# Kernel tuning notes

Hardware: AMD Instinct MI355X
Metric: run time of the kernel (lower is better)

The kernel has to match this reference:

```python
import jax, jax.numpy as jnp
import numpy as np
from jax import lax

IN_CH = 256
NUM_CLASSES = 21
ROI = 7
SCALE = 1.0 / 32
SR = 2  # sampling_ratio
B = 2
NPROP = 128
FH = FW = 32
IMG = 1024
SCORE_THRESH = 0.05
NMS_THRESH = 0.5
MAX_DET = 100


def setup_inputs() -> dict:
    key = jax.random.key(0)
    ks = jax.random.split(key, 10)
    features = jax.random.normal(ks[0], (B, IN_CH, FH, FW), jnp.float32)
    x1 = jax.random.uniform(ks[1], (B, NPROP), minval=0.0, maxval=IMG - 160.0)
    y1 = jax.random.uniform(ks[2], (B, NPROP), minval=0.0, maxval=IMG - 160.0)
    w = jax.random.uniform(ks[3], (B, NPROP), minval=32.0, maxval=160.0)
    h = jax.random.uniform(ks[4], (B, NPROP), minval=32.0, maxval=160.0)
    proposals = jnp.stack([x1, y1, x1 + w, y1 + h], axis=-1)  # [B, NPROP, 4]
    img_sizes = jnp.full((B, 2), IMG, dtype=jnp.int32)  # (h, w)
    feat_dim = IN_CH * ROI * ROI

    def kaiming(k, shape):
        return jax.random.normal(k, shape, jnp.float32) * np.float32(np.sqrt(2.0 / shape[1]))

    W1 = kaiming(ks[5], (1024, feat_dim)); b1 = jnp.zeros((1024,), jnp.float32)
    W2 = kaiming(ks[6], (1024, 1024)); b2 = jnp.zeros((1024,), jnp.float32)
    Wc = jax.random.normal(ks[7], (NUM_CLASSES, 1024), jnp.float32) * 0.01
    bc = jnp.zeros((NUM_CLASSES,), jnp.float32)
    Wb = jax.random.normal(ks[8], (NUM_CLASSES * 4, 1024), jnp.float32) * 0.001
    bb = jnp.zeros((NUM_CLASSES * 4,), jnp.float32)
    return dict(features=features, proposals=proposals, img_sizes=img_sizes,
                W1=W1, b1=b1, W2=W2, b2=b2, Wc=Wc, bc=bc, Wb=Wb, bb=bb)


def roi_align(features, bidx, rois):
    """torchvision-style RoIAlign (aligned=False), spatial_scale=SCALE, sampling_ratio=SR.
    features [B,C,H,W], bidx [N] int, rois [N,4] -> [N, C*ROI*ROI] (channel-major flatten)."""
    Bf, C, H, W = features.shape
    x1 = rois[:, 0] * SCALE; y1 = rois[:, 1] * SCALE
    x2 = rois[:, 2] * SCALE; y2 = rois[:, 3] * SCALE
    rw = jnp.maximum(x2 - x1, 1.0); rh = jnp.maximum(y2 - y1, 1.0)
    bw = rw / ROI; bh = rh / ROI
    # per-bin sample offsets: [ROI, SR]
    g = jnp.arange(ROI, dtype=jnp.float32)[:, None] + (jnp.arange(SR, dtype=jnp.float32)[None, :] + 0.5) / SR
    ys = y1[:, None, None] + g[None] * bh[:, None, None]  # [N, ROI, SR]
    xs = x1[:, None, None] + g[None] * bw[:, None, None]  # [N, ROI, SR]
    y = ys[:, :, :, None, None]  # [N,ph,sy,1,1]
    x = xs[:, None, None, :, :]  # [N,1,1,pw,sx]
    inb = (y >= -1.0) & (y <= H) & (x >= -1.0) & (x <= W)  # [N,ph,sy,pw,sx]
    yc = jnp.clip(y, 0.0, H - 1.0); xc = jnp.clip(x, 0.0, W - 1.0)
    y0f = jnp.floor(yc); x0f = jnp.floor(xc)
    y0 = y0f.astype(jnp.int32); x0 = x0f.astype(jnp.int32)
    y1i = jnp.minimum(y0 + 1, H - 1); x1i = jnp.minimum(x0 + 1, W - 1)
    ly = yc - y0f; lx = xc - x0f
    hy = 1.0 - ly; hx = 1.0 - lx
    b = bidx[:, None, None, None, None]
    # gather four corners: advanced indices broadcast -> [N,ph,sy,pw,sx,C]
    f00 = features[b, :, y0, x0]
    f01 = features[b, :, y0, x1i]
    f10 = features[b, :, y1i, x0]
    f11 = features[b, :, y1i, x1i]
    val = ((hy * hx)[..., None] * f00 + (hy * lx)[..., None] * f01
           + (ly * hx)[..., None] * f10 + (ly * lx)[..., None] * f11)
    val = val * inb[..., None]
    pooled = val.mean(axis=(2, 4))            # [N, ph, pw, C]
    pooled = jnp.transpose(pooled, (0, 3, 1, 2))  # [N, C, ph, pw] (torch layout)
    return pooled.reshape(pooled.shape[0], -1)


def decode_boxes(deltas, props):
    pw = props[..., 2] - props[..., 0]
    ph = props[..., 3] - props[..., 1]
    px = props[..., 0] + pw / 2
    py = props[..., 1] + ph / 2
    cx = px + deltas[..., 0] * pw
    cy = py + deltas[..., 1] * ph
    w = pw * jnp.exp(deltas[..., 2])
    h = ph * jnp.exp(deltas[..., 3])
    return jnp.stack([cx - w / 2, cy - h / 2, cx + w / 2, cy + h / 2], axis=-1)


def nms_fixed(boxes, scores, valid, iou_thresh, max_out):
    """Greedy NMS with fixed shapes. Returns (indices[max_out], ok_mask[max_out])."""
    M = scores.shape[0]
    s = jnp.where(valid, scores, -jnp.inf)
    order = jnp.argsort(-s)
    b = boxes[order]; v = valid[order]
    bx1, by1, bx2, by2 = b[:, 0], b[:, 1], b[:, 2], b[:, 3]
    area = (bx2 - bx1) * (by2 - by1)
    idxs = jnp.arange(M)

    def body(i, keep):
        xi1 = jnp.maximum(bx1[i], bx1); yi1 = jnp.maximum(by1[i], by1)
        xi2 = jnp.minimum(bx2[i], bx2); yi2 = jnp.minimum(by2[i], by2)
        inter = jnp.maximum(xi2 - xi1, 0.0) * jnp.maximum(yi2 - yi1, 0.0)
        iou = inter / (area[i] + area - inter + 1e-9)
        suppress = (iou > iou_thresh) & (idxs > i)
        return jnp.where(keep[i], keep & ~suppress, keep)

    keep = lax.fori_loop(0, M, body, v)
    pos = jnp.where(keep, idxs, M)
    take = jnp.sort(pos)[:max_out]
    ok = take < M
    take = jnp.where(ok, take, 0)
    return order[take], ok


def postprocess_image(probs, reg, props, img_hw):
    Ncls = probs.shape[1]
    scores = probs[:, 1:]                    # [N, C-1] (skip background)
    deltas = reg[:, 1:, :]                   # [N, C-1, 4]
    boxes = decode_boxes(deltas, props[:, None, :])  # [N, C-1, 4]
    h = img_hw[0].astype(boxes.dtype); w = img_hw[1].astype(boxes.dtype)
    boxes = jnp.stack([jnp.clip(boxes[..., 0], 0.0, w), jnp.clip(boxes[..., 1], 0.0, h),
                       jnp.clip(boxes[..., 2], 0.0, w), jnp.clip(boxes[..., 3], 0.0, h)], axis=-1)
    labels = jnp.broadcast_to(jnp.arange(1, Ncls, dtype=jnp.int32)[None, :], scores.shape)
    fb = boxes.reshape(-1, 4); fs = scores.reshape(-1); fl = labels.reshape(-1)
    valid = fs > SCORE_THRESH
    maxc = jnp.max(jnp.where(valid, jnp.max(fb, axis=1), 0.0))
    off = fl.astype(fb.dtype) * (maxc + 1.0)
    zero = jnp.zeros_like(off)
    fb_off = fb + jnp.stack([off, zero, off, zero], axis=-1)
    idx, ok = nms_fixed(fb_off, fs, valid, NMS_THRESH, MAX_DET)
    m = ok.astype(fb.dtype)
    return fb[idx] * m[:, None], fs[idx] * m, fl[idx] * ok.astype(jnp.int32)


def reference(features, proposals, img_sizes, W1, b1, W2, b2, Wc, bc, Wb, bb):
    Bn, NP = proposals.shape[0], proposals.shape[1]
    bidx = jnp.repeat(jnp.arange(Bn, dtype=jnp.int32), NP)
    props_flat = proposals.reshape(-1, 4)
    roi_feats = roi_align(features, bidx, props_flat)       # [N, C*49]
    x = jax.nn.relu(roi_feats @ W1.T + b1)
    x = jax.nn.relu(x @ W2.T + b2)
    cls_logits = x @ Wc.T + bc                              # [N, NUM_CLASSES]
    box_reg = (x @ Wb.T + bb).reshape(-1, NUM_CLASSES, 4)   # [N, NUM_CLASSES, 4]
    probs = jax.nn.softmax(cls_logits, axis=-1)
    out_b, out_s, out_l = [], [], []
    for i in range(Bn):
        p = probs[i * NP:(i + 1) * NP]
        r = box_reg[i * NP:(i + 1) * NP]
        bi, si, li = postprocess_image(p, r, proposals[i], img_sizes[i])
        out_b.append(bi); out_s.append(si); out_l.append(li)
    return jnp.stack(out_b), jnp.stack(out_s), jnp.stack(out_l)
```

## Files before the change

kernel.cpp:

```cpp
#include <hip/hip_runtime.h>
#include <math.h>

#define IN_CH   256
#define NCLS    21
#define ROIW    7
#define NPROP   128
#define BATCH   2
#define NROI    (BATCH*NPROP)
#define FEAT_DIM (IN_CH*ROIW*ROIW)
#define HID     1024
#define NCAND   (NPROP*(NCLS-1))
#define MAXDET  100
#define SCORE_T 0.05f
#define NMS_T   0.5f

__global__ __launch_bounds__(256) void transpose_feat(const float* __restrict__ feat,
                                                      float* __restrict__ ft) {
    int img = blockIdx.z;
    int cb = blockIdx.y;
    int pb = blockIdx.x;
    __shared__ float t[32][33];
    int tx = threadIdx.x & 31, ty = threadIdx.x >> 5;
#pragma unroll
    for (int i = 0; i < 4; ++i) {
        int c = ty + i * 8;
        t[c][tx] = feat[(size_t)img * 262144 + (size_t)(cb * 32 + c) * 1024 + pb * 32 + tx];
    }
    __syncthreads();
#pragma unroll
    for (int i = 0; i < 4; ++i) {
        int p = ty + i * 8;
        ft[(size_t)img * 262144 + (size_t)(pb * 32 + p) * 256 + cb * 32 + tx] = t[tx][p];
    }
}

__global__ __launch_bounds__(256) void roi_align_tr(const float* __restrict__ ft,
                                                    const float* __restrict__ props,
                                                    float* __restrict__ out) {
    int n = blockIdx.x >> 1;
    int half = blockIdx.x & 1;
    int img = n / NPROP;
    int q0 = half ? 25 : 0;
    int nq = half ? 24 : 25;
    const float* pr = props + n * 4;
    float x1 = pr[0] * 0.03125f, y1 = pr[1] * 0.03125f;
    float x2 = pr[2] * 0.03125f, y2 = pr[3] * 0.03125f;
    float rw = fmaxf(x2 - x1, 1.0f), rh = fmaxf(y2 - y1, 1.0f);
    float bw = rw / 7.0f, bh = rh / 7.0f;
    int cg = threadIdx.x & 63;
    int qg = threadIdx.x >> 6;
    __shared__ float tile[25][260];
    const float* base = ft + (size_t)img * 262144 + cg * 4;
    for (int j = qg; j < nq; j += 4) {
        int q = q0 + j;
        int iy = q / 7, ix = q % 7;
        float ax = 0.f, ay = 0.f, az = 0.f, aw = 0.f;
#pragma unroll
        for (int s = 0; s < 4; ++s) {
            int sy = s >> 1, sx = s & 1;
            float gy = (float)iy + ((float)sy + 0.5f) / 2.0f;
            float gx = (float)ix + ((float)sx + 0.5f) / 2.0f;
            float y = y1 + gy * bh;
            float x = x1 + gx * bw;
            bool inb = (y >= -1.0f) && (y <= 32.0f) && (x >= -1.0f) && (x <= 32.0f);
            float yc = fminf(fmaxf(y, 0.0f), 31.0f);
            float xc = fminf(fmaxf(x, 0.0f), 31.0f);
            float y0f = floorf(yc), x0f = floorf(xc);
            int y0 = (int)y0f, x0i = (int)x0f;
            int y1i = min(y0 + 1, 31), x1i = min(x0i + 1, 31);
            float ly = yc - y0f, lx = xc - x0f;
            float hy = 1.0f - ly, hx = 1.0f - lx;
            float wg = inb ? 1.0f : 0.0f;
            float w00 = hy * hx * wg, w01 = hy * lx * wg, w10 = ly * hx * wg, w11 = ly * lx * wg;
            float4 f00 = *(const float4*)(base + (size_t)(y0 * 32 + x0i) * 256);
            float4 f01 = *(const float4*)(base + (size_t)(y0 * 32 + x1i) * 256);
            float4 f10 = *(const float4*)(base + (size_t)(y1i * 32 + x0i) * 256);
            float4 f11 = *(const float4*)(base + (size_t)(y1i * 32 + x1i) * 256);
            ax += w00 * f00.x + w01 * f01.x + w10 * f10.x + w11 * f11.x;
            ay += w00 * f00.y + w01 * f01.y + w10 * f10.y + w11 * f11.y;
            az += w00 * f00.z + w01 * f01.z + w10 * f10.z + w11 * f11.z;
            aw += w00 * f00.w + w01 * f01.w + w10 * f10.w + w11 * f11.w;
        }
        *(float4*)&tile[j][cg * 4] = make_float4(ax * 0.25f, ay * 0.25f, az * 0.25f, aw * 0.25f);
    }
    __syncthreads();
    float* ob = out + (size_t)n * FEAT_DIM + q0;
    int tid = threadIdx.x;
    if (half == 0) {
        for (int i = tid; i < 256 * 25; i += 256) {
            int c = i / 25, ql = i % 25;
            ob[c * 49 + ql] = tile[ql][c];
        }
    } else {
        for (int i = tid; i < 256 * 24; i += 256) {
            int c = i / 24, ql = i % 24;
            ob[c * 49 + ql] = tile[ql][c];
        }
    }
}

#define GBM 128
#define GBN 128
#define GBK 16
__global__ __launch_bounds__(256) void gemm_tn_part(const float* __restrict__ A,
                                                    const float* __restrict__ Wt,
                                                    float* __restrict__ Cp,
                                                    int Nr, int Mo, int K) {
    const int S = gridDim.z;
    const int kchunk = K / S;
    const int k0 = blockIdx.z * kchunk;
    const int n0 = blockIdx.y * GBM;
    const int j0 = blockIdx.x * GBN;
    __shared__ float As[GBK][GBM + 4];
    __shared__ float Ws[GBK][GBN + 4];
    const int tid = threadIdx.x;
    const int tx = tid & 15;
    const int ty = tid >> 4;
    const int r0 = tx << 2;
    const int c0 = ty << 2;
    const int srow = tid >> 1;
    const int skk = (tid & 1) << 3;
    float acc[8][8];
#pragma unroll
    for (int r = 0; r < 8; ++r)
#pragma unroll
        for (int c = 0; c < 8; ++c) acc[r][c] = 0.0f;

    const int iters = kchunk / GBK;
    const float* Abase = A + (size_t)(n0 + srow) * K + skk;
    const float* Wbase = Wt + (size_t)(j0 + srow) * K + skk;
    float4 pa0 = *(const float4*)(Abase + k0);
    float4 pa1 = *(const float4*)(Abase + k0 + 4);
    float4 pw0 = *(const float4*)(Wbase + k0);
    float4 pw1 = *(const float4*)(Wbase + k0 + 4);

#pragma unroll 1
    for (int it = 0; it < iters; ++it) {
        __syncthreads();
        As[skk + 0][srow] = pa0.x; As[skk + 1][srow] = pa0.y; As[skk + 2][srow] = pa0.z; As[skk + 3][srow] = pa0.w;
        As[skk + 4][srow] = pa1.x; As[skk + 5][srow] = pa1.y; As[skk + 6][srow] = pa1.z; As[skk + 7][srow] = pa1.w;
        Ws[skk + 0][srow] = pw0.x; Ws[skk + 1][srow] = pw0.y; Ws[skk + 2][srow] = pw0.z; Ws[skk + 3][srow] = pw0.w;
        Ws[skk + 4][srow] = pw1.x; Ws[skk + 5][srow] = pw1.y; Ws[skk + 6][srow] = pw1.z; Ws[skk + 7][srow] = pw1.w;
        __syncthreads();
        if (it + 1 < iters) {
            int kc = k0 + (it + 1) * GBK;
            pa0 = *(const float4*)(Abase + kc);
            pa1 = *(const float4*)(Abase + kc + 4);
            pw0 = *(const float4*)(Wbase + kc);
            pw1 = *(const float4*)(Wbase + kc + 4);
        }
        float4 fa0[2], fa1[2], fw0[2], fw1[2];
        fa0[0] = *(const float4*)&As[0][r0];
        fa1[0] = *(const float4*)&As[0][r0 + 64];
        fw0[0] = *(const float4*)&Ws[0][c0];
        fw1[0] = *(const float4*)&Ws[0][c0 + 64];
#pragma unroll
        for (int k = 0; k < GBK; ++k) {
            const int cur = k & 1, nxt = cur ^ 1;
            if (k + 1 < GBK) {
                fa0[nxt] = *(const float4*)&As[k + 1][r0];
                fa1[nxt] = *(const float4*)&As[k + 1][r0 + 64];
                fw0[nxt] = *(const float4*)&Ws[k + 1][c0];
                fw1[nxt] = *(const float4*)&Ws[k + 1][c0 + 64];
            }
            float a[8] = {fa0[cur].x, fa0[cur].y, fa0[cur].z, fa0[cur].w,
                          fa1[cur].x, fa1[cur].y, fa1[cur].z, fa1[cur].w};
            float w[8] = {fw0[cur].x, fw0[cur].y, fw0[cur].z, fw0[cur].w,
                          fw1[cur].x, fw1[cur].y, fw1[cur].z, fw1[cur].w};
#pragma unroll
            for (int r = 0; r < 8; ++r)
#pragma unroll
                for (int c = 0; c < 8; ++c)
                    acc[r][c] = fmaf(a[r], w[c], acc[r][c]);
        }
    }
#pragma unroll
    for (int r = 0; r < 8; ++r) {
        int gr = n0 + ((r < 4) ? (r0 + r) : (r0 + 64 + r - 4));
        float* o = Cp + ((size_t)blockIdx.z * Nr + gr) * Mo + j0;
        *(float4*)(o + c0)      = make_float4(acc[r][0], acc[r][1], acc[r][2], acc[r][3]);
        *(float4*)(o + c0 + 64) = make_float4(acc[r][4], acc[r][5], acc[r][6], acc[r][7]);
    }
}

__global__ __launch_bounds__(256) void reduce_bias_relu(const float* __restrict__ Cp,
                                                        const float* __restrict__ bias,
                                                        float* __restrict__ X,
                                                        int Nr, int Mo, int S) {
    int idx = blockIdx.x * 256 + threadIdx.x;
    int total = (Nr * Mo) >> 2;
    if (idx >= total) return;
    int e = idx << 2;
    int j = e % Mo;
    float4 s = make_float4(0.f, 0.f, 0.f, 0.f);
    for (int ss = 0; ss < S; ++ss) {
        float4 c = *(const float4*)(Cp + (size_t)ss * Nr * Mo + e);
        s.x += c.x; s.y += c.y; s.z += c.z; s.w += c.w;
    }
    float4 b = *(const float4*)(bias + j);
    s.x = fmaxf(s.x + b.x, 0.f); s.y = fmaxf(s.y + b.y, 0.f);
    s.z = fmaxf(s.z + b.z, 0.f); s.w = fmaxf(s.w + b.w, 0.f);
    *(float4*)(X + e) = s;
}

__global__ __launch_bounds__(256) void heads_cand_k(const float* __restrict__ Cp2,
                                                    const float* __restrict__ b2,
                                                    const float* __restrict__ Wc, const float* __restrict__ bc,
                                                    const float* __restrict__ Wb, const float* __restrict__ bb,
                                                    const float* __restrict__ props,
                                                    const int* __restrict__ img_sizes,
                                                    float* __restrict__ cbox,
                                                    float* __restrict__ csc,
                                                    unsigned long long* __restrict__ ckey,
                                                    int* __restrict__ vcount) {
    int n = blockIdx.x;
    int tid = threadIdx.x;
    if (n == 0 && tid < 2) vcount[tid] = 0;
    __shared__ float xs[HID];
    __shared__ float lg[NCLS];
    __shared__ float bs[84];
    __shared__ float ssum;
    {
        int e = n * HID + tid * 4;
        float4 s = make_float4(0.f, 0.f, 0.f, 0.f);
#pragma unroll
        for (int ss = 0; ss < 16; ++ss) {
            float4 c = *(const float4*)(Cp2 + (size_t)ss * (NROI * HID) + e);
            s.x += c.x; s.y += c.y; s.z += c.z; s.w += c.w;
        }
        float4 b = *(const float4*)(b2 + tid * 4);
        s.x = fmaxf(s.x + b.x, 0.f); s.y = fmaxf(s.y + b.y, 0.f);
        s.z = fmaxf(s.z + b.z, 0.f); s.w = fmaxf(s.w + b.w, 0.f);
        *(float4*)&xs[tid * 4] = s;
    }
    __syncthreads();
    int wave = tid >> 6, lane = tid & 63;
    for (int h = wave; h < 105; h += 4) {
        const float* w = (h < 21) ? (Wc + (size_t)h * HID) : (Wb + (size_t)(h - 21) * HID);
        float acc = 0.0f;
#pragma unroll
        for (int k0 = 0; k0 < HID; k0 += 256) {
            float4 wv = *(const float4*)(w + k0 + lane * 4);
            float4 xv = *(const float4*)&xs[k0 + lane * 4];
            acc = fmaf(wv.x, xv.x, acc);
            acc = fmaf(wv.y, xv.y, acc);
            acc = fmaf(wv.z, xv.z, acc);
            acc = fmaf(wv.w, xv.w, acc);
        }
#pragma unroll
        for (int m = 32; m; m >>= 1) acc += __shfl_xor(acc, m, 64);
        if (lane == 0) {
            if (h < 21) lg[h] = acc + bc[h];
            else bs[h - 21] = acc + bb[h - 21];
        }
    }
    __syncthreads();
    if (tid == 0) {
        float m = lg[0];
        for (int c = 1; c < 21; ++c) m = fmaxf(m, lg[c]);
        float s = 0.0f;
        for (int c = 0; c < 21; ++c) { float e = expf(lg[c] - m); lg[c] = e; s += e; }
        ssum = s;
    }
    __syncthreads();
    if (tid < 20) {
        int c = tid + 1;
        int img = n / NPROP;
        float s = lg[c] / ssum;
        const float* pr = props + n * 4;
        float pw = pr[2] - pr[0], ph = pr[3] - pr[1];
        float px = pr[0] + pw * 0.5f, py = pr[1] + ph * 0.5f;
        const float* d = &bs[c * 4];
        float cx = px + d[0] * pw;
        float cy = py + d[1] * ph;
        float w = pw * expf(d[2]);
        float h = ph * expf(d[3]);
        float bx1 = cx - w * 0.5f, by1 = cy - h * 0.5f, bx2 = cx + w * 0.5f, by2 = cy + h * 0.5f;
        float Wi = (float)img_sizes[img * 2 + 1], Hi = (float)img_sizes[img * 2 + 0];
        bx1 = fminf(fmaxf(bx1, 0.f), Wi); by1 = fminf(fmaxf(by1, 0.f), Hi);
        bx2 = fminf(fmaxf(bx2, 0.f), Wi); by2 = fminf(fmaxf(by2, 0.f), Hi);
        int t = n * 20 + tid;
        *(float4*)(cbox + (size_t)t * 4) = make_float4(bx1, by1, bx2, by2);
        csc[t] = s;
        bool valid = s > SCORE_T;
        unsigned int sb = __float_as_uint(s);
        int m = t - img * NCAND;
        ckey[t] = valid ? (((unsigned long long)sb << 32) | (unsigned int)(NCAND - 1 - m)) : 0ull;
    }
}

__global__ __launch_bounds__(256) void rank_k(const float* __restrict__ cbox,
                                              const float* __restrict__ csc,
                                              const unsigned long long* __restrict__ ckey,
                                              float* __restrict__ sbox, float* __restrict__ ssc,
                                              int* __restrict__ sm, int* __restrict__ vcount) {
    int img = blockIdx.x / 40;
    int seg = blockIdx.x % 40;
    int base = img * NCAND;
    int lm = threadIdx.x & 63;
    int chunk = threadIdx.x >> 6;
    int m = seg * 64 + lm;
    __shared__ __align__(16) unsigned long long keys[NCAND];
    for (int j = threadIdx.x; j < NCAND; j += 256) keys[j] = ckey[base + j];
    unsigned long long mykey = ckey[base + m];
    float s = csc[base + m];
    bool valid = s > SCORE_T;
    __syncthreads();
    const ulonglong2* kp = (const ulonglong2*)&keys[chunk * 640];
    int r = 0;
#pragma unroll 4
    for (int j = 0; j < 320; ++j) {
        ulonglong2 kk = kp[j];
        r += (kk.x > mykey) ? 1 : 0;
        r += (kk.y > mykey) ? 1 : 0;
    }
    __shared__ int part[4][64];
    part[chunk][lm] = r;
    __syncthreads();
    if (chunk == 0) {
        int rank = part[0][lm] + part[1][lm] + part[2][lm] + part[3][lm];
        if (valid) {
            int o = base + rank;
            *(float4*)(sbox + (size_t)o * 4) = *(const float4*)(cbox + (size_t)(base + m) * 4);
            ssc[o] = s;
            sm[o] = m;
        }
    }
    int cnt = __syncthreads_count((chunk == 0) && valid);
    if (threadIdx.x == 0) atomicAdd(&vcount[img], cnt);
}

__global__ __launch_bounds__(64) void nms_k(const int* __restrict__ sm,
                                            const float* __restrict__ sbox,
                                            const int* __restrict__ vcount,
                                            int* __restrict__ skeep) {
    int bid = blockIdx.x;
    int img = bid / 20;
    int cls = bid % 20 + 1;
    int V = vcount[img];
    __shared__ float lx1[128], ly1[128], lx2[128], ly2[128];
    __shared__ int lpos[128];
    __shared__ int lcnt;
    __shared__ int keepL[128];
    int lane = threadIdx.x;
    if (lane == 0) lcnt = 0;
    __syncthreads();
    for (int p0 = 0; p0 < V; p0 += 64) {
        int p = p0 + lane;
        bool pred = false;
        if (p < V) {
            int m = sm[img * NCAND + p];
            pred = (m % 20 + 1) == cls;
        }
        unsigned long long mask = __ballot(pred);
        int base = lcnt;
        if (pred) {
            int idx = base + __popcll(mask & ((1ull << lane) - 1ull));
            const float* bx = sbox + (size_t)(img * NCAND + (p0 + lane)) * 4;
            lx1[idx] = bx[0]; ly1[idx] = bx[1]; lx2[idx] = bx[2]; ly2[idx] = bx[3];
            lpos[idx] = p0 + lane;
        }
        __syncthreads();
        if (lane == 0) lcnt += (int)__popcll(mask);
        __syncthreads();
    }
    int C = lcnt;
    for (int j = lane; j < 128; j += 64) keepL[j] = 1;
    __syncthreads();
    for (int i = 0; i < C; ++i) {
        __syncthreads();
        if (keepL[i] == 0) continue;
        float X1 = lx1[i], Y1 = ly1[i], X2 = lx2[i], Y2 = ly2[i];
        float ai = (X2 - X1) * (Y2 - Y1);
        for (int j = i + 1 + lane; j < C; j += 64) {
            if (keepL[j]) {
                float xi1 = fmaxf(X1, lx1[j]);
                float yi1 = fmaxf(Y1, ly1[j]);
                float xi2 = fminf(X2, lx2[j]);
                float yi2 = fminf(Y2, ly2[j]);
                float inter = fmaxf(xi2 - xi1, 0.f) * fmaxf(yi2 - yi1, 0.f);
                float aj = (lx2[j] - lx1[j]) * (ly2[j] - ly1[j]);
                float iou = inter / (ai + aj - inter + 1e-9f);
                if (iou > NMS_T) keepL[j] = 0;
            }
        }
    }
    __syncthreads();
    for (int j = lane; j < C; j += 64) skeep[img * NCAND + lpos[j]] = keepL[j];
}

__global__ __launch_bounds__(256) void write_k(const float* __restrict__ sbox,
                                               const float* __restrict__ ssc,
                                               const int* __restrict__ sm,
                                               const int* __restrict__ skeep,
                                               const int* __restrict__ vcount,
                                               float* __restrict__ out) {
    int img = blockIdx.x;
    int tid = threadIdx.x;
    float* ob = out + img * MAXDET * 4;
    float* os = out + BATCH * MAXDET * 4 + img * MAXDET;
    float* ol = out + BATCH * MAXDET * 5 + img * MAXDET;
    for (int i = tid; i < MAXDET * 4; i += 256) ob[i] = 0.0f;
    for (int i = tid; i < MAXDET; i += 256) { os[i] = 0.0f; ol[i] = 0.0f; }
    __syncthreads();
    int V = vcount[img];
    int chunk = (V + 255) / 256;
    int lo = tid * chunk, hi = min(lo + chunk, V);
    int cnt = 0;
    for (int p = lo; p < hi; ++p) cnt += skeep[img * NCAND + p];
    __shared__ int cs[256];
    __shared__ int pre[256];
    cs[tid] = cnt;
    __syncthreads();
    if (tid == 0) {
        int run = 0;
        for (int t = 0; t < 256; ++t) { pre[t] = run; run += cs[t]; }
    }
    __syncthreads();
    int r = pre[tid];
    for (int p = lo; p < hi; ++p) {
        if (skeep[img * NCAND + p]) {
            if (r < MAXDET) {
                const float* bx = sbox + (size_t)(img * NCAND + p) * 4;
                ob[r * 4 + 0] = bx[0]; ob[r * 4 + 1] = bx[1];
                ob[r * 4 + 2] = bx[2]; ob[r * 4 + 3] = bx[3];
                os[r] = ssc[img * NCAND + p];
                ol[r] = (float)(sm[img * NCAND + p] % 20 + 1);
            }
            ++r;
        }
    }
}

extern "C" void kernel_launch(void* const* d_in, const int* in_sizes, int n_in,
                              void* d_out, int out_size, void* d_ws, size_t ws_size,
                              hipStream_t stream) {
    const float* features  = (const float*)d_in[0];
    const float* proposals = (const float*)d_in[1];
    const int*   img_sizes = (const int*)d_in[2];
    const float* W1 = (const float*)d_in[3];
    const float* b1 = (const float*)d_in[4];
    const float* W2 = (const float*)d_in[5];
    const float* b2 = (const float*)d_in[6];
    const float* Wc = (const float*)d_in[7];
    const float* bc = (const float*)d_in[8];
    const float* Wb = (const float*)d_in[9];
    const float* bb = (const float*)d_in[10];
    float* out = (float*)d_out;

    float* ws = (float*)d_ws;
    float* roi   = ws;
    float* x1    = roi + 3211264;
    float* cpart = x1 + 262144;
    float* featT = cpart;
    float* cbox  = cpart + 16 * 262144;
    float* csc   = cbox + 20480;
    unsigned long long* ckey = (unsigned long long*)(csc + 5120);
    float* sbox  = csc + 5120 + 10240;
    float* ssc   = sbox + 20480;
    int*   sm    = (int*)(ssc + 5120);
    int*   skeep = sm + 5120;
    int*   vcnt  = skeep + 5120;

    hipLaunchKernelGGL(transpose_feat, dim3(32, 8, 2), dim3(256), 0, stream, features, featT);
    hipLaunchKernelGGL(roi_align_tr, dim3(NROI * 2), dim3(256), 0, stream, featT, proposals, roi);
    hipLaunchKernelGGL(gemm_tn_part, dim3(8, 2, 16), dim3(256), 0, stream, roi, W1, cpart, NROI, HID, FEAT_DIM);
    hipLaunchKernelGGL(reduce_bias_relu, dim3(256), dim3(256), 0, stream, cpart, b1, x1, NROI, HID, 16);
    hipLaunchKernelGGL(gemm_tn_part, dim3(8, 2, 16), dim3(256), 0, stream, x1, W2, cpart, NROI, HID, HID);
    hipLaunchKernelGGL(heads_cand_k, dim3(NROI), dim3(256), 0, stream, cpart, b2, Wc, bc, Wb, bb,
                       proposals, img_sizes, cbox, csc, ckey, vcnt);
    hipLaunchKernelGGL(rank_k, dim3(80), dim3(256), 0, stream, cbox, csc, ckey, sbox, ssc, sm, vcnt);
    hipLaunchKernelGGL(nms_k, dim3(BATCH * 20), dim3(64), 0, stream, sm, sbox, vcnt, skeep);
    hipLaunchKernelGGL(write_k, dim3(BATCH), dim3(256), 0, stream, sbox, ssc, sm, skeep, vcnt, out);
}
```

Measured before the change: 319.9 us.

## Replace LDS-tiled GEMM with register-direct K-major GEMM using transposed activations

Activations are transposed to K-major layout (a new transpose kernel for the RoI features, and the reduce/bias/ReLU kernel now writes its output transposed). The GEMM then drops shared memory and barriers entirely: each thread loads its A fragments straight from global memory as float4 and its W rows as float4 runs of 4 k-values. This removes LDS traffic and syncs, but adds an extra pass over the 12.8MB RoI tensor. It also relies on L1/L2 for reuse, since each thread's strided W row reads are uncoalesced across the wave and A reads are repeated across blocks.

```diff
diff --git a/kernel.cpp b/kernel.cpp
--- a/kernel.cpp
+++ b/kernel.cpp
@@ -31,6 +31,25 @@
     for (int i = 0; i < 4; ++i) {
         int p = ty + i * 8;
         ft[(size_t)img * 262144 + (size_t)(pb * 32 + p) * 256 + cb * 32 + tx] = t[tx][p];
+    }
+}
+
+__global__ __launch_bounds__(256) void transpose_mat(const float* __restrict__ in,
+                                                     float* __restrict__ out,
+                                                     int R, int C) {
+    __shared__ float t[32][33];
+    int cb = blockIdx.x * 32, rb = blockIdx.y * 32;
+    int tx = threadIdx.x & 31, ty = threadIdx.x >> 5;
+#pragma unroll
+    for (int i = 0; i < 4; ++i) {
+        int r = rb + ty + i * 8;
+        t[ty + i * 8][tx] = in[(size_t)r * C + cb + tx];
+    }
+    __syncthreads();
+#pragma unroll
+    for (int i = 0; i < 4; ++i) {
+        int c = cb + ty + i * 8;
+        out[(size_t)c * R + rb + tx] = t[tx][ty + i * 8];
     }
 }
 
@@ -99,74 +118,49 @@
     }
 }
 
-#define GBM 128
-#define GBN 128
-#define GBK 16
-__global__ __launch_bounds__(256) void gemm_tn_part(const float* __restrict__ A,
-                                                    const float* __restrict__ Wt,
-                                                    float* __restrict__ Cp,
-                                                    int Nr, int Mo, int K) {
+__global__ __launch_bounds__(256) void gemm_kt(const float* __restrict__ At,
+                                               const float* __restrict__ W,
+                                               float* __restrict__ Cp,
+                                               int Nr, int Mo, int K) {
     const int S = gridDim.z;
     const int kchunk = K / S;
     const int k0 = blockIdx.z * kchunk;
-    const int n0 = blockIdx.y * GBM;
-    const int j0 = blockIdx.x * GBN;
-    __shared__ float As[GBK][GBM + 4];
-    __shared__ float Ws[GBK][GBN + 4];
+    const int n0 = blockIdx.y * 128;
+    const int j0 = blockIdx.x * 128;
     const int tid = threadIdx.x;
     const int tx = tid & 15;
     const int ty = tid >> 4;
     const int r0 = tx << 2;
     const int c0 = ty << 2;
-    const int srow = tid >> 1;
-    const int skk = (tid & 1) << 3;
     float acc[8][8];
 #pragma unroll
     for (int r = 0; r < 8; ++r)
 #pragma unroll
         for (int c = 0; c < 8; ++c) acc[r][c] = 0.0f;
 
-    const int iters = kchunk / GBK;
-    const float* Abase = A + (size_t)(n0 + srow) * K + skk;
-    const float* Wbase = Wt + (size_t)(j0 + srow) * K + skk;
-    float4 pa0 = *(const float4*)(Abase + k0);
-    float4 pa1 = *(const float4*)(Abase + k0 + 4);
-    float4 pw0 = *(const float4*)(Wbase + k0);
-    float4 pw1 = *(const float4*)(Wbase + k0 + 4);
+    const float* a_base = At + (size_t)k0 * Nr + n0 + r0;
+    const float* w0base = W + (size_t)(j0 + c0) * K + k0;
+    const float* w1base = W + (size_t)(j0 + c0 + 64) * K + k0;
+    const int runs = kchunk >> 2;
 
 #pragma unroll 1
-    for (int it = 0; it < iters; ++it) {
-        __syncthreads();
-        As[skk + 0][srow] = pa0.x; As[skk + 1][srow] = pa0.y; As[skk + 2][srow] = pa0.z; As[skk + 3][srow] = pa0.w;
-        As[skk + 4][srow] = pa1.x; As[skk + 5][srow] = pa1.y; As[skk + 6][srow] = pa1.z; As[skk + 7][srow] = pa1.w;
-        Ws[skk + 0][srow] = pw0.x; Ws[skk + 1][srow] = pw0.y; Ws[skk + 2][srow] = pw0.z; Ws[skk + 3][srow] = pw0.w;
-        Ws[skk + 4][srow] = pw1.x; Ws[skk + 5][srow] = pw1.y; Ws[skk + 6][srow] = pw1.z; Ws[skk + 7][srow] = pw1.w;
-        __syncthreads();
-        if (it + 1 < iters) {
-            int kc = k0 + (it + 1) * GBK;
-            pa0 = *(const float4*)(Abase + kc);
-            pa1 = *(const float4*)(Abase + kc + 4);
-            pw0 = *(const float4*)(Wbase + kc);
-            pw1 = *(const float4*)(Wbase + kc + 4);
-        }
-        float4 fa0[2], fa1[2], fw0[2], fw1[2];
-        fa0[0] = *(const float4*)&As[0][r0];
-        fa1[0] = *(const float4*)&As[0][r0 + 64];
-        fw0[0] = *(const float4*)&Ws[0][c0];
-        fw1[0] = *(const float4*)&Ws[0][c0 + 64];
-#pragma unroll
-        for (int k = 0; k < GBK; ++k) {
-            const int cur = k & 1, nxt = cur ^ 1;
-            if (k + 1 < GBK) {
-                fa0[nxt] = *(const float4*)&As[k + 1][r0];
-                fa1[nxt] = *(const float4*)&As[k + 1][r0 + 64];
-                fw0[nxt] = *(const float4*)&Ws[k + 1][c0];
-                fw1[nxt] = *(const float4*)&Ws[k + 1][c0 + 64];
-            }
-            float a[8] = {fa0[cur].x, fa0[cur].y, fa0[cur].z, fa0[cur].w,
-                          fa1[cur].x, fa1[cur].y, fa1[cur].z, fa1[cur].w};
-            float w[8] = {fw0[cur].x, fw0[cur].y, fw0[cur].z, fw0[cur].w,
-                          fw1[cur].x, fw1[cur].y, fw1[cur].z, fw1[cur].w};
+    for (int run = 0; run < runs; ++run) {
+        float4 wr[8];
+#pragma unroll
+        for (int c = 0; c < 4; ++c) {
+            wr[c]     = *(const float4*)(w0base + (size_t)c * K + run * 4);
+            wr[c + 4] = *(const float4*)(w1base + (size_t)c * K + run * 4);
+        }
+#pragma unroll
+        for (int k = 0; k < 4; ++k) {
+            const float* ap = a_base + (size_t)(run * 4 + k) * Nr;
+            float4 a0 = *(const float4*)(ap);
+            float4 a1 = *(const float4*)(ap + 64);
+            float a[8] = {a0.x, a0.y, a0.z, a0.w, a1.x, a1.y, a1.z, a1.w};
+            float w[8];
+#pragma unroll
+            for (int c = 0; c < 8; ++c)
+                w[c] = (k == 0) ? wr[c].x : (k == 1) ? wr[c].y : (k == 2) ? wr[c].z : wr[c].w;
 #pragma unroll
             for (int r = 0; r < 8; ++r)
 #pragma unroll
@@ -183,24 +177,27 @@
     }
 }
 
-__global__ __launch_bounds__(256) void reduce_bias_relu(const float* __restrict__ Cp,
-                                                        const float* __restrict__ bias,
-                                                        float* __restrict__ X,
-                                                        int Nr, int Mo, int S) {
-    int idx = blockIdx.x * 256 + threadIdx.x;
-    int total = (Nr * Mo) >> 2;
-    if (idx >= total) return;
-    int e = idx << 2;
-    int j = e % Mo;
-    float4 s = make_float4(0.f, 0.f, 0.f, 0.f);
-    for (int ss = 0; ss < S; ++ss) {
-        float4 c = *(const float4*)(Cp + (size_t)ss * Nr * Mo + e);
-        s.x += c.x; s.y += c.y; s.z += c.z; s.w += c.w;
-    }
-    float4 b = *(const float4*)(bias + j);
-    s.x = fmaxf(s.x + b.x, 0.f); s.y = fmaxf(s.y + b.y, 0.f);
-    s.z = fmaxf(s.z + b.z, 0.f); s.w = fmaxf(s.w + b.w, 0.f);
-    *(float4*)(X + e) = s;
+__global__ __launch_bounds__(256) void reduce_bias_relu_t(const float* __restrict__ Cp,
+                                                          const float* __restrict__ bias,
+                                                          float* __restrict__ XT,
+                                                          int Nr, int Mo, int S) {
+    __shared__ float t[32][33];
+    int jb = blockIdx.x * 32, nb = blockIdx.y * 32;
+    int tx = threadIdx.x & 31, ty = threadIdx.x >> 5;
+#pragma unroll
+    for (int i = 0; i < 4; ++i) {
+        int nl = ty + i * 8;
+        int e = (nb + nl) * Mo + jb + tx;
+        float s = 0.0f;
+        for (int ss = 0; ss < S; ++ss) s += Cp[(size_t)ss * Nr * Mo + e];
+        t[nl][tx] = fmaxf(s + bias[jb + tx], 0.0f);
+    }
+    __syncthreads();
+#pragma unroll
+    for (int i = 0; i < 4; ++i) {
+        int jl = ty + i * 8;
+        XT[(size_t)(jb + jl) * Nr + nb + tx] = t[tx][jl];
+    }
 }
 
 __global__ __launch_bounds__(256) void heads_cand_k(const float* __restrict__ Cp2,
@@ -450,8 +447,9 @@
 
     float* ws = (float*)d_ws;
     float* roi   = ws;
-    float* x1    = roi + 3211264;
-    float* cpart = x1 + 262144;
+    float* roiT  = roi + 3211264;
+    float* x1T   = roiT + 3211264;
+    float* cpart = x1T + 262144;
     float* featT = cpart;
     float* cbox  = cpart + 16 * 262144;
     float* csc   = cbox + 20480;
@@ -464,9 +462,12 @@
 
     hipLaunchKernelGGL(transpose_feat, dim3(32, 8, 2), dim3(256), 0, stream, features, featT);
     hipLaunchKernelGGL(roi_align_tr, dim3(NROI * 2), dim3(256), 0, stream, featT, proposals, roi);
-    hipLaunchKernelGGL(gemm_tn_part, dim3(8, 2, 16), dim3(256), 0, stream, roi, W1, cpart, NROI, HID, FEAT_DIM);
-    hipLaunchKernelGGL(reduce_bias_relu, dim3(256), dim3(256), 0, stream, cpart, b1, x1, NROI, HID, 16);
-    hipLaunchKernelGGL(gemm_tn_part, dim3(8, 2, 16), dim3(256), 0, stream, x1, W2, cpart, NROI, HID, HID);
+    hipLaunchKernelGGL(transpose_mat, dim3(FEAT_DIM / 32, NROI / 32), dim3(256), 0, stream,
+                       roi, roiT, NROI, FEAT_DIM);
+    hipLaunchKernelGGL(gemm_kt, dim3(8, 2, 16), dim3(256), 0, stream, roiT, W1, cpart, NROI, HID, FEAT_DIM);
+    hipLaunchKernelGGL(reduce_bias_relu_t, dim3(HID / 32, NROI / 32), dim3(256), 0, stream,
+                       cpart, b1, x1T, NROI, HID, 16);
+    hipLaunchKernelGGL(gemm_kt, dim3(8, 2, 16), dim3(256), 0, stream, x1T, W2, cpart, NROI, HID, HID);
     hipLaunchKernelGGL(heads_cand_k, dim3(NROI), dim3(256), 0, stream, cpart, b2, Wc, bc, Wb, bb,
                        proposals, img_sizes, cbox, csc, ckey, vcnt);
     hipLaunchKernelGGL(rank_k, dim3(80), dim3(256), 0, stream, cbox, csc, ckey, sbox, ssc, sm, vcnt);
```

Result: slower. 686.5 us (+114.6%).

## Add 256-row FC1 GEMM kernel so W1 is read once, raise split-K to 28

Applied to the files above, without the earlier changes.

Adds a dedicated FC1 GEMM kernel whose block covers all 256 ROI rows and 128 output columns with a 16x8 per-thread accumulator. Each W1 tile is then loaded once instead of once per 128-row block, which halves W1 global traffic. Split-K goes from 16 to 28 (K=12544 divides into 448-element chunks) to keep 224 blocks in flight and fill the GPU. The trade-off is higher register pressure from 128 accumulators, launch_bounds(256,1), and more partial sums for the reduce kernel to read. The shared-memory register double-buffering in the generic GEMM is also removed.

```diff
diff --git a/kernel.cpp b/kernel.cpp
--- a/kernel.cpp
+++ b/kernel.cpp
@@ -13,6 +13,7 @@
 #define MAXDET  100
 #define SCORE_T 0.05f
 #define NMS_T   0.5f
+#define S_FC1   28
 
 __global__ __launch_bounds__(256) void transpose_feat(const float* __restrict__ feat,
                                                       float* __restrict__ ft) {
@@ -99,6 +100,87 @@
     }
 }
 
+#define G2K 16
+__global__ __launch_bounds__(256, 1) void gemm_fc1(const float* __restrict__ A,
+                                                   const float* __restrict__ Wt,
+                                                   float* __restrict__ Cp,
+                                                   int Nr, int Mo, int K) {
+    const int S = gridDim.y;
+    const int kchunk = K / S;
+    const int k0 = blockIdx.y * kchunk;
+    const int j0 = blockIdx.x * 128;
+    __shared__ float As[G2K][256 + 4];
+    __shared__ float Ws[G2K][128 + 4];
+    const int tid = threadIdx.x;
+    const int tx = tid & 15;
+    const int ty = tid >> 4;
+    const int r0 = tx << 2;
+    const int c0 = ty << 2;
+    const int rA = tid;
+    const int rW = tid >> 1;
+    const int kW = (tid & 1) << 3;
+    float acc[16][8];
+#pragma unroll
+    for (int r = 0; r < 16; ++r)
+#pragma unroll
+        for (int c = 0; c < 8; ++c) acc[r][c] = 0.0f;
+
+    const int iters = kchunk / G2K;
+    const float* Ab = A + (size_t)rA * K;
+    const float* Wb = Wt + (size_t)(j0 + rW) * K + kW;
+    float4 pa0 = *(const float4*)(Ab + k0);
+    float4 pa1 = *(const float4*)(Ab + k0 + 4);
+    float4 pa2 = *(const float4*)(Ab + k0 + 8);
+    float4 pa3 = *(const float4*)(Ab + k0 + 12);
+    float4 pw0 = *(const float4*)(Wb + k0);
+    float4 pw1 = *(const float4*)(Wb + k0 + 4);
+
+#pragma unroll 1
+    for (int it = 0; it < iters; ++it) {
+        __syncthreads();
+        As[0][rA] = pa0.x;  As[1][rA] = pa0.y;  As[2][rA] = pa0.z;  As[3][rA] = pa0.w;
+        As[4][rA] = pa1.x;  As[5][rA] = pa1.y;  As[6][rA] = pa1.z;  As[7][rA] = pa1.w;
+        As[8][rA] = pa2.x;  As[9][rA] = pa2.y;  As[10][rA] = pa2.z; As[11][rA] = pa2.w;
+        As[12][rA] = pa3.x; As[13][rA] = pa3.y; As[14][rA] = pa3.z; As[15][rA] = pa3.w;
+        Ws[kW + 0][rW] = pw0.x; Ws[kW + 1][rW] = pw0.y; Ws[kW + 2][rW] = pw0.z; Ws[kW + 3][rW] = pw0.w;
+        Ws[kW + 4][rW] = pw1.x; Ws[kW + 5][rW] = pw1.y; Ws[kW + 6][rW] = pw1.z; Ws[kW + 7][rW] = pw1.w;
+        __syncthreads();
+        if (it + 1 < iters) {
+            int kc = k0 + (it + 1) * G2K;
+            pa0 = *(const float4*)(Ab + kc);
+            pa1 = *(const float4*)(Ab + kc + 4);
+            pa2 = *(const float4*)(Ab + kc + 8);
+            pa3 = *(const float4*)(Ab + kc + 12);
+            pw0 = *(const float4*)(Wb + kc);
+            pw1 = *(const float4*)(Wb + kc + 4);
+        }
+#pragma unroll
+        for (int k = 0; k < G2K; ++k) {
+            float4 a0 = *(const float4*)&As[k][r0];
+            float4 a1 = *(const float4*)&As[k][r0 + 64];
+            float4 a2 = *(const float4*)&As[k][r0 + 128];
+            float4 a3 = *(const float4*)&As[k][r0 + 192];
+            float4 u0 = *(const float4*)&Ws[k][c0];
+            float4 u1 = *(const float4*)&Ws[k][c0 + 64];
+            float a[16] = {a0.x, a0.y, a0.z, a0.w, a1.x, a1.y, a1.z, a1.w,
+                           a2.x, a2.y, a2.z, a2.w, a3.x, a3.y, a3.z, a3.w};
+            float w[8] = {u0.x, u0.y, u0.z, u0.w, u1.x, u1.y, u1.z, u1.w};
+#pragma unroll
+            for (int r = 0; r < 16; ++r)
+#pragma unroll
+                for (int c = 0; c < 8; ++c)
+                    acc[r][c] = fmaf(a[r], w[c], acc[r][c]);
+        }
+    }
+#pragma unroll
+    for (int r = 0; r < 16; ++r) {
+        int gr = r0 + (r >> 2) * 64 + (r & 3);
+        float* o = Cp + ((size_t)blockIdx.y * Nr + gr) * Mo + j0;
+        *(float4*)(o + c0)      = make_float4(acc[r][0], acc[r][1], acc[r][2], acc[r][3]);
+        *(float4*)(o + c0 + 64) = make_float4(acc[r][4], acc[r][5], acc[r][6], acc[r][7]);
+    }
+}
+
 #define GBM 128
 #define GBN 128
 #define GBK 16
@@ -149,24 +231,14 @@
             pw0 = *(const float4*)(Wbase + kc);
             pw1 = *(const float4*)(Wbase + kc + 4);
         }
-        float4 fa0[2], fa1[2], fw0[2], fw1[2];
-        fa0[0] = *(const float4*)&As[0][r0];
-        fa1[0] = *(const float4*)&As[0][r0 + 64];
-        fw0[0] = *(const float4*)&Ws[0][c0];
-        fw1[0] = *(const float4*)&Ws[0][c0 + 64];
 #pragma unroll
         for (int k = 0; k < GBK; ++k) {
-            const int cur = k & 1, nxt = cur ^ 1;
-            if (k + 1 < GBK) {
-                fa0[nxt] = *(const float4*)&As[k + 1][r0];
-                fa1[nxt] = *(const float4*)&As[k + 1][r0 + 64];
-                fw0[nxt] = *(const float4*)&Ws[k + 1][c0];
-                fw1[nxt] = *(const float4*)&Ws[k + 1][c0 + 64];
-            }
-            float a[8] = {fa0[cur].x, fa0[cur].y, fa0[cur].z, fa0[cur].w,
-                          fa1[cur].x, fa1[cur].y, fa1[cur].z, fa1[cur].w};
-            float w[8] = {fw0[cur].x, fw0[cur].y, fw0[cur].z, fw0[cur].w,
-                          fw1[cur].x, fw1[cur].y, fw1[cur].z, fw1[cur].w};
+            float4 t0 = *(const float4*)&As[k][r0];
+            float4 t1 = *(const float4*)&As[k][r0 + 64];
+            float4 u0 = *(const float4*)&Ws[k][c0];
+            float4 u1 = *(const float4*)&Ws[k][c0 + 64];
+            float a[8] = {t0.x, t0.y, t0.z, t0.w, t1.x, t1.y, t1.z, t1.w};
+            float w[8] = {u0.x, u0.y, u0.z, u0.w, u1.x, u1.y, u1.z, u1.w};
 #pragma unroll
             for (int r = 0; r < 8; ++r)
 #pragma unroll
@@ -453,7 +525,7 @@
     float* x1    = roi + 3211264;
     float* cpart = x1 + 262144;
     float* featT = cpart;
-    float* cbox  = cpart + 16 * 262144;
+    float* cbox  = cpart + (size_t)S_FC1 * 262144;
     float* csc   = cbox + 20480;
     unsigned long long* ckey = (unsigned long long*)(csc + 5120);
     float* sbox  = csc + 5120 + 10240;
@@ -464,8 +536,8 @@
 
     hipLaunchKernelGGL(transpose_feat, dim3(32, 8, 2), dim3(256), 0, stream, features, featT);
     hipLaunchKernelGGL(roi_align_tr, dim3(NROI * 2), dim3(256), 0, stream, featT, proposals, roi);
-    hipLaunchKernelGGL(gemm_tn_part, dim3(8, 2, 16), dim3(256), 0, stream, roi, W1, cpart, NROI, HID, FEAT_DIM);
-    hipLaunchKernelGGL(reduce_bias_relu, dim3(256), dim3(256), 0, stream, cpart, b1, x1, NROI, HID, 16);
+    hipLaunchKernelGGL(gemm_fc1, dim3(8, S_FC1), dim3(256), 0, stream, roi, W1, cpart, NROI, HID, FEAT_DIM);
+    hipLaunchKernelGGL(reduce_bias_relu, dim3(256), dim3(256), 0, stream, cpart, b1, x1, NROI, HID, S_FC1);
     hipLaunchKernelGGL(gemm_tn_part, dim3(8, 2, 16), dim3(256), 0, stream, x1, W2, cpart, NROI, HID, HID);
     hipLaunchKernelGGL(heads_cand_k, dim3(NROI), dim3(256), 0, stream, cpart, b2, Wc, bc, Wb, bb,
                        proposals, img_sizes, cbox, csc, ckey, vcnt);
```

New measurement: 324.3 us. Within noise of the previous version (+1.4%).
